# Optimization experiments

Measured on AMD Instinct MI355X. Metric: run time of the kernel, lower is better.

The kernel has to match this reference:

```python
import jax, jax.numpy as jnp
import numpy as np


def setup_inputs() -> dict:
    key = jax.random.key(0)
    k1, k2, k3 = jax.random.split(key, 3)
    B, M, J = 4096, 64, 24  # batch, n_max_markers, n_joints
    points = jax.random.normal(k1, (B, M, 3), dtype=jnp.float32)
    weight = jax.random.uniform(k2, (B, M, J), dtype=jnp.float32)  # positive soft weights
    offset = jax.random.normal(k3, (B, M, J, 3), dtype=jnp.float32)
    return {"points": points, "weight": weight, "offset": offset}


def reference(points, weight, offset):
    # P: per-joint marker offsets (B, J, 3, M); Q: world marker positions (B, 1, 3, M)
    P = jnp.transpose(offset, (0, 2, 3, 1))
    Q = jnp.transpose(points, (0, 2, 1))[:, None]
    w = jnp.transpose(weight, (0, 2, 1))[:, :, None]  # (B, J, 1, M)

    wsum = jnp.sum(w, axis=-1)                   # (B, J, 1)
    P_ = jnp.sum(P * w, axis=-1) / wsum          # (B, J, 3) weighted centroid of offsets
    Q_ = jnp.sum(Q * w, axis=-1) / wsum          # (B, J, 3) weighted centroid of markers

    X = P - P_[..., None]                        # (B, J, 3, M)
    Y = Q - Q_[..., None]                        # (B, J, 3, M) via broadcast

    # Cross-covariance S = X @ Y^T (NOTE: original multiplies un-weighted centered coords)
    S = jnp.einsum('bjdm,bjem->bjde', X, Y)      # (B, J, 3, 3)

    U, _, Vh = jnp.linalg.svd(S)
    V = jnp.swapaxes(Vh, -1, -2)
    Ut = jnp.swapaxes(U, -1, -2)
    det = jnp.linalg.det(jnp.matmul(V, Ut))      # (B, J) reflection correction
    Ut = Ut.at[..., -1, :].multiply(det[..., None])
    R = jnp.matmul(V, Ut)                        # (B, J, 3, 3) optimal rotation
    t = Q_[..., None] - jnp.matmul(R, P_[..., None])  # (B, J, 3, 1)
    return R, t
```

## Files before the change

### kernel.cpp

```cpp
#include <hip/hip_runtime.h>


constexpr int M = 64;
constexpr int J = 24;
constexpr int NACC = 22;
constexpr int NWS  = 15;

constexpr int WSTR = 27;
constexpr int OSTR = 73;
constexpr int WLEN = M * WSTR;
constexpr int OLEN = M * OSTR;
constexpr int PLEN = M * 3;
constexpr int KSP  = 8;
constexpr int RED  = KSP * J;

__global__ __launch_bounds__(256) void accum_kernel(
    const float* __restrict__ points,
    const float* __restrict__ weight,
    const float* __restrict__ offset,
    float* __restrict__ ws,
    int bj_total)
{
    __shared__ float smem[WLEN + OLEN + PLEN];
    float* lw = smem;
    float* lo = smem + WLEN;
    float* lp = smem + WLEN + OLEN;
    float* red = smem + WLEN;

    const int t = threadIdx.x;
    const int b = blockIdx.x;

    const float4* wg = (const float4*)(weight + (size_t)b * (M * J));
    for (int idx = t; idx < (M * J) / 4; idx += 256) {
        float4 v = wg[idx];
        int g0 = idx * 4;
#pragma unroll
        for (int c = 0; c < 4; ++c) {
            int g = g0 + c;
            int m = g / J, r = g - m * J;
            lw[m * WSTR + r] = (&v.x)[c];
        }
    }
    const float4* og = (const float4*)(offset + (size_t)b * (M * J * 3));
    for (int idx = t; idx < (M * J * 3) / 4; idx += 256) {
        float4 v = og[idx];
        int g0 = idx * 4;
#pragma unroll
        for (int c = 0; c < 4; ++c) {
            int g = g0 + c;
            int m = g / (J * 3), r = g - m * (J * 3);
            lo[m * OSTR + r] = (&v.x)[c];
        }
    }
    const float4* pg = (const float4*)(points + (size_t)b * (M * 3));
    if (t < PLEN / 4) ((float4*)lp)[t] = pg[t];

    __syncthreads();

    float acc[NACC];
#pragma unroll
    for (int n = 0; n < NACC; ++n) acc[n] = 0.0f;

    if (t < KSP * J) {
        const int j = t % J;
        const int k = t / J;
#pragma unroll
        for (int i = 0; i < M / KSP; ++i) {
            const int m = k * (M / KSP) + i;
            float w  = lw[m * WSTR + j];
            float o0 = lo[m * OSTR + j * 3 + 0];
            float o1 = lo[m * OSTR + j * 3 + 1];
            float o2 = lo[m * OSTR + j * 3 + 2];
            float p0 = lp[m * 3 + 0];
            float p1 = lp[m * 3 + 1];
            float p2 = lp[m * 3 + 2];
            acc[0] += w;
            acc[1] = fmaf(w, o0, acc[1]);  acc[2] = fmaf(w, o1, acc[2]);  acc[3] = fmaf(w, o2, acc[3]);
            acc[4] = fmaf(w, p0, acc[4]);  acc[5] = fmaf(w, p1, acc[5]);  acc[6] = fmaf(w, p2, acc[6]);
            acc[7] += o0; acc[8] += o1; acc[9] += o2;
            acc[10] += p0; acc[11] += p1; acc[12] += p2;
            acc[13] = fmaf(o0, p0, acc[13]); acc[14] = fmaf(o0, p1, acc[14]); acc[15] = fmaf(o0, p2, acc[15]);
            acc[16] = fmaf(o1, p0, acc[16]); acc[17] = fmaf(o1, p1, acc[17]); acc[18] = fmaf(o1, p2, acc[18]);
            acc[19] = fmaf(o2, p0, acc[19]); acc[20] = fmaf(o2, p1, acc[20]); acc[21] = fmaf(o2, p2, acc[21]);
        }
    }

    __syncthreads();
    if (t < KSP * J) {
#pragma unroll
        for (int n = 0; n < NACC; ++n) red[n * RED + t] = acc[n];
    }
    __syncthreads();

    if (t < J) {
        float T[NACC];
#pragma unroll
        for (int n = 0; n < NACC; ++n) {
            float s = 0.0f;
#pragma unroll
            for (int k = 0; k < KSP; ++k) s += red[n * RED + k * J + t];
            T[n] = s;
        }
        const float inv = __builtin_amdgcn_rcpf(T[0]);
        const float cP0 = T[1] * inv, cP1 = T[2] * inv, cP2 = T[3] * inv;
        const float cQ0 = T[4] * inv, cQ1 = T[5] * inv, cQ2 = T[6] * inv;
        const float To0 = T[7], To1 = T[8], To2 = T[9];
        const float Tp0 = T[10], Tp1 = T[11], Tp2 = T[12];
        const float fM = (float)M;
        float Sv[NWS];
        Sv[0] = T[13] - cP0 * Tp0 - cQ0 * To0 + fM * cP0 * cQ0;
        Sv[1] = T[14] - cP0 * Tp1 - cQ1 * To0 + fM * cP0 * cQ1;
        Sv[2] = T[15] - cP0 * Tp2 - cQ2 * To0 + fM * cP0 * cQ2;
        Sv[3] = T[16] - cP1 * Tp0 - cQ0 * To1 + fM * cP1 * cQ0;
        Sv[4] = T[17] - cP1 * Tp1 - cQ1 * To1 + fM * cP1 * cQ1;
        Sv[5] = T[18] - cP1 * Tp2 - cQ2 * To1 + fM * cP1 * cQ2;
        Sv[6] = T[19] - cP2 * Tp0 - cQ0 * To2 + fM * cP2 * cQ0;
        Sv[7] = T[20] - cP2 * Tp1 - cQ1 * To2 + fM * cP2 * cQ1;
        Sv[8] = T[21] - cP2 * Tp2 - cQ2 * To2 + fM * cP2 * cQ2;
        Sv[9] = cP0;  Sv[10] = cP1; Sv[11] = cP2;
        Sv[12] = cQ0; Sv[13] = cQ1; Sv[14] = cQ2;
        const int bj = b * J + t;
#pragma unroll
        for (int n = 0; n < NWS; ++n) ws[(size_t)n * bj_total + bj] = Sv[n];
    }
}

template<int P, int Q>
__device__ __forceinline__ void jrot(float A[4][4], float V[4][4]) {
    float apq = A[P][Q];
    float theta = (A[Q][Q] - A[P][P]) * __builtin_amdgcn_rcpf(2.0f * apq);
    float t = __builtin_amdgcn_rcpf(fabsf(theta) + __builtin_amdgcn_sqrtf(fmaf(theta, theta, 1.0f)));
    t = (theta < 0.0f) ? -t : t;
    t = (apq == 0.0f) ? 0.0f : t;
    float c = __builtin_amdgcn_rsqf(fmaf(t, t, 1.0f));
    float s = t * c;
#pragma unroll
    for (int k = 0; k < 4; ++k) {
        float akp = A[k][P], akq = A[k][Q];
        A[k][P] = c * akp - s * akq;
        A[k][Q] = s * akp + c * akq;
    }
#pragma unroll
    for (int k = 0; k < 4; ++k) {
        float apk = A[P][k], aqk = A[Q][k];
        A[P][k] = c * apk - s * aqk;
        A[Q][k] = s * apk + c * aqk;
        float vkp = V[k][P], vkq = V[k][Q];
        V[k][P] = c * vkp - s * vkq;
        V[k][Q] = s * vkp + c * vkq;
    }
}

__device__ __forceinline__ void horn_solve(
    float S00, float S01, float S02, float S10, float S11, float S12,
    float S20, float S21, float S22,
    float cP0, float cP1, float cP2, float cQ0, float cQ1, float cQ2,
    float* __restrict__ Rout, float* __restrict__ tout)
{
    float A[4][4], V[4][4];
    A[0][0] = S00 + S11 + S22;
    A[0][1] = A[1][0] = S12 - S21;
    A[0][2] = A[2][0] = S20 - S02;
    A[0][3] = A[3][0] = S01 - S10;
    A[1][1] = S00 - S11 - S22;
    A[1][2] = A[2][1] = S01 + S10;
    A[1][3] = A[3][1] = S02 + S20;
    A[2][2] = -S00 + S11 - S22;
    A[2][3] = A[3][2] = S12 + S21;
    A[3][3] = -S00 - S11 + S22;
#pragma unroll
    for (int r = 0; r < 4; ++r)
#pragma unroll
        for (int c = 0; c < 4; ++c)
            V[r][c] = (r == c) ? 1.0f : 0.0f;

#pragma unroll 1
    for (int sweep = 0; sweep < 6; ++sweep) {
        jrot<0, 1>(A, V); jrot<0, 2>(A, V); jrot<0, 3>(A, V);
        jrot<1, 2>(A, V); jrot<1, 3>(A, V); jrot<2, 3>(A, V);
    }

    float best = A[0][0];
    float qw = V[0][0], qx = V[1][0], qy = V[2][0], qz = V[3][0];
#pragma unroll
    for (int i = 1; i < 4; ++i) {
        bool better = A[i][i] > best;
        best = better ? A[i][i] : best;
        qw = better ? V[0][i] : qw;
        qx = better ? V[1][i] : qx;
        qy = better ? V[2][i] : qy;
        qz = better ? V[3][i] : qz;
    }
    float nrm = __builtin_amdgcn_rsqf(qw * qw + qx * qx + qy * qy + qz * qz);
    qw *= nrm; qx *= nrm; qy *= nrm; qz *= nrm;

    float R00 = 1.f - 2.f * (qy * qy + qz * qz);
    float R01 = 2.f * (qx * qy - qw * qz);
    float R02 = 2.f * (qx * qz + qw * qy);
    float R10 = 2.f * (qx * qy + qw * qz);
    float R11 = 1.f - 2.f * (qx * qx + qz * qz);
    float R12 = 2.f * (qy * qz - qw * qx);
    float R20 = 2.f * (qx * qz - qw * qy);
    float R21 = 2.f * (qy * qz + qw * qx);
    float R22 = 1.f - 2.f * (qx * qx + qy * qy);

    Rout[0] = R00; Rout[1] = R01; Rout[2] = R02;
    Rout[3] = R10; Rout[4] = R11; Rout[5] = R12;
    Rout[6] = R20; Rout[7] = R21; Rout[8] = R22;
    tout[0] = cQ0 - (R00 * cP0 + R01 * cP1 + R02 * cP2);
    tout[1] = cQ1 - (R10 * cP0 + R11 * cP1 + R12 * cP2);
    tout[2] = cQ2 - (R20 * cP0 + R21 * cP1 + R22 * cP2);
}

__global__ __launch_bounds__(64) void solve_kernel(
    const float* __restrict__ ws, float* __restrict__ out, int bj_total)
{
    int tid = blockIdx.x * 64 + threadIdx.x;
    if (tid >= bj_total) return;
    float Sv[NWS];
#pragma unroll
    for (int n = 0; n < NWS; ++n) Sv[n] = ws[(size_t)n * bj_total + tid];
    float Rr[9], tr[3];
    horn_solve(Sv[0], Sv[1], Sv[2], Sv[3], Sv[4], Sv[5], Sv[6], Sv[7], Sv[8],
               Sv[9], Sv[10], Sv[11], Sv[12], Sv[13], Sv[14], Rr, tr);
    float* Rout = out + (size_t)tid * 9;
#pragma unroll
    for (int n = 0; n < 9; ++n) Rout[n] = Rr[n];
    float* tout = out + (size_t)bj_total * 9 + (size_t)tid * 3;
    tout[0] = tr[0]; tout[1] = tr[1]; tout[2] = tr[2];
}

__global__ __launch_bounds__(256) void fused_kernel(
    const float* __restrict__ points, const float* __restrict__ weight,
    const float* __restrict__ offset, float* __restrict__ out, int bj_total)
{
    int tid = blockIdx.x * blockDim.x + threadIdx.x;
    if (tid >= bj_total) return;
    int b = tid / J, j = tid - b * J;
    const float* wq = weight + (size_t)b * M * J + j;
    const float* oq = offset + ((size_t)b * M * J + j) * 3;
    const float* pq = points + (size_t)b * M * 3;
    float a[NACC];
#pragma unroll
    for (int n = 0; n < NACC; ++n) a[n] = 0.0f;
#pragma unroll 4
    for (int m = 0; m < M; ++m) {
        float w = wq[m * J];
        float o0 = oq[m * (J * 3) + 0], o1 = oq[m * (J * 3) + 1], o2 = oq[m * (J * 3) + 2];
        float p0 = pq[m * 3 + 0], p1 = pq[m * 3 + 1], p2 = pq[m * 3 + 2];
        a[0] += w;
        a[1] = fmaf(w, o0, a[1]); a[2] = fmaf(w, o1, a[2]); a[3] = fmaf(w, o2, a[3]);
        a[4] = fmaf(w, p0, a[4]); a[5] = fmaf(w, p1, a[5]); a[6] = fmaf(w, p2, a[6]);
        a[7] += o0; a[8] += o1; a[9] += o2;
        a[10] += p0; a[11] += p1; a[12] += p2;
        a[13] = fmaf(o0, p0, a[13]); a[14] = fmaf(o0, p1, a[14]); a[15] = fmaf(o0, p2, a[15]);
        a[16] = fmaf(o1, p0, a[16]); a[17] = fmaf(o1, p1, a[17]); a[18] = fmaf(o1, p2, a[18]);
        a[19] = fmaf(o2, p0, a[19]); a[20] = fmaf(o2, p1, a[20]); a[21] = fmaf(o2, p2, a[21]);
    }
    float inv = __builtin_amdgcn_rcpf(a[0]);
    float cP0 = a[1] * inv, cP1 = a[2] * inv, cP2 = a[3] * inv;
    float cQ0 = a[4] * inv, cQ1 = a[5] * inv, cQ2 = a[6] * inv;
    const float fM = (float)M;
    float S00 = a[13] - cP0 * a[10] - cQ0 * a[7] + fM * cP0 * cQ0;
    float S01 = a[14] - cP0 * a[11] - cQ1 * a[7] + fM * cP0 * cQ1;
    float S02 = a[15] - cP0 * a[12] - cQ2 * a[7] + fM * cP0 * cQ2;
    float S10 = a[16] - cP1 * a[10] - cQ0 * a[8] + fM * cP1 * cQ0;
    float S11 = a[17] - cP1 * a[11] - cQ1 * a[8] + fM * cP1 * cQ1;
    float S12 = a[18] - cP1 * a[12] - cQ2 * a[8] + fM * cP1 * cQ2;
    float S20 = a[19] - cP2 * a[10] - cQ0 * a[9] + fM * cP2 * cQ0;
    float S21 = a[20] - cP2 * a[11] - cQ1 * a[9] + fM * cP2 * cQ1;
    float S22 = a[21] - cP2 * a[12] - cQ2 * a[9] + fM * cP2 * cQ2;
    float Rr[9], tr[3];
    horn_solve(S00, S01, S02, S10, S11, S12, S20, S21, S22,
               cP0, cP1, cP2, cQ0, cQ1, cQ2, Rr, tr);
    float* Rout = out + (size_t)tid * 9;
#pragma unroll
    for (int n = 0; n < 9; ++n) Rout[n] = Rr[n];
    float* tout = out + (size_t)bj_total * 9 + (size_t)tid * 3;
    tout[0] = tr[0]; tout[1] = tr[1]; tout[2] = tr[2];
}

extern "C" void kernel_launch(void* const* d_in, const int* in_sizes, int n_in,
                              void* d_out, int out_size, void* d_ws, size_t ws_size,
                              hipStream_t stream) {
    const float* points = (const float*)d_in[0];
    const float* weight = (const float*)d_in[1];
    const float* offset = (const float*)d_in[2];
    float* out = (float*)d_out;

    int B = in_sizes[0] / (M * 3);
    int bj_total = B * J;

    size_t need = (size_t)NWS * bj_total * sizeof(float);
    if (ws_size >= need) {
        accum_kernel<<<B, 256, 0, stream>>>(points, weight, offset, (float*)d_ws, bj_total);
        solve_kernel<<<(bj_total + 63) / 64, 64, 0, stream>>>((const float*)d_ws, out, bj_total);
    } else {
        fused_kernel<<<(bj_total + 255) / 256, 256, 0, stream>>>(points, weight, offset, out, bj_total);
    }
}
```

Baseline: 153.7 us.

## Fuse accumulation and Horn eigen-solve into one kernel with LDS-staged output

Result: slower. 187.1 us (+21.7%).

```diff
diff --git a/kernel.cpp b/kernel.cpp
--- a/kernel.cpp
+++ b/kernel.cpp
@@ -4,7 +4,6 @@
 constexpr int M = 64;
 constexpr int J = 24;
 constexpr int NACC = 22;
-constexpr int NWS  = 15;
 
 constexpr int WSTR = 27;
 constexpr int OSTR = 73;
@@ -14,11 +13,37 @@
 constexpr int KSP  = 8;
 constexpr int RED  = KSP * J;
 
-__global__ __launch_bounds__(256) void accum_kernel(
+template<int P, int Q>
+__device__ __forceinline__ void jrot(float A[4][4], float V[4][4]) {
+    float apq = A[P][Q];
+    float theta = (A[Q][Q] - A[P][P]) * __builtin_amdgcn_rcpf(2.0f * apq);
+    float t = __builtin_amdgcn_rcpf(fabsf(theta) + __builtin_amdgcn_sqrtf(fmaf(theta, theta, 1.0f)));
+    t = (theta < 0.0f) ? -t : t;
+    t = (apq == 0.0f) ? 0.0f : t;
+    float c = __builtin_amdgcn_rsqf(fmaf(t, t, 1.0f));
+    float s = t * c;
+#pragma unroll
+    for (int k = 0; k < 4; ++k) {
+        float akp = A[k][P], akq = A[k][Q];
+        A[k][P] = c * akp - s * akq;
+        A[k][Q] = s * akp + c * akq;
+    }
+#pragma unroll
+    for (int k = 0; k < 4; ++k) {
+        float apk = A[P][k], aqk = A[Q][k];
+        A[P][k] = c * apk - s * aqk;
+        A[Q][k] = s * apk + c * aqk;
+        float vkp = V[k][P], vkq = V[k][Q];
+        V[k][P] = c * vkp - s * vkq;
+        V[k][Q] = s * vkp + c * vkq;
+    }
+}
+
+__global__ __launch_bounds__(256) void kabsch_fused(
     const float* __restrict__ points,
     const float* __restrict__ weight,
     const float* __restrict__ offset,
-    float* __restrict__ ws,
+    float* __restrict__ out,
     int bj_total)
 {
     __shared__ float smem[WLEN + OLEN + PLEN];
@@ -26,6 +51,7 @@
     float* lo = smem + WLEN;
     float* lp = smem + WLEN + OLEN;
     float* red = smem + WLEN;
+    float* ost = smem;
 
     const int t = threadIdx.x;
     const int b = blockIdx.x;
@@ -107,177 +133,81 @@
         const float To0 = T[7], To1 = T[8], To2 = T[9];
         const float Tp0 = T[10], Tp1 = T[11], Tp2 = T[12];
         const float fM = (float)M;
-        float Sv[NWS];
-        Sv[0] = T[13] - cP0 * Tp0 - cQ0 * To0 + fM * cP0 * cQ0;
-        Sv[1] = T[14] - cP0 * Tp1 - cQ1 * To0 + fM * cP0 * cQ1;
-        Sv[2] = T[15] - cP0 * Tp2 - cQ2 * To0 + fM * cP0 * cQ2;
-        Sv[3] = T[16] - cP1 * Tp0 - cQ0 * To1 + fM * cP1 * cQ0;
-        Sv[4] = T[17] - cP1 * Tp1 - cQ1 * To1 + fM * cP1 * cQ1;
-        Sv[5] = T[18] - cP1 * Tp2 - cQ2 * To1 + fM * cP1 * cQ2;
-        Sv[6] = T[19] - cP2 * Tp0 - cQ0 * To2 + fM * cP2 * cQ0;
-        Sv[7] = T[20] - cP2 * Tp1 - cQ1 * To2 + fM * cP2 * cQ1;
-        Sv[8] = T[21] - cP2 * Tp2 - cQ2 * To2 + fM * cP2 * cQ2;
-        Sv[9] = cP0;  Sv[10] = cP1; Sv[11] = cP2;
-        Sv[12] = cQ0; Sv[13] = cQ1; Sv[14] = cQ2;
-        const int bj = b * J + t;
-#pragma unroll
-        for (int n = 0; n < NWS; ++n) ws[(size_t)n * bj_total + bj] = Sv[n];
-    }
-}
-
-template<int P, int Q>
-__device__ __forceinline__ void jrot(float A[4][4], float V[4][4]) {
-    float apq = A[P][Q];
-    float theta = (A[Q][Q] - A[P][P]) * __builtin_amdgcn_rcpf(2.0f * apq);
-    float t = __builtin_amdgcn_rcpf(fabsf(theta) + __builtin_amdgcn_sqrtf(fmaf(theta, theta, 1.0f)));
-    t = (theta < 0.0f) ? -t : t;
-    t = (apq == 0.0f) ? 0.0f : t;
-    float c = __builtin_amdgcn_rsqf(fmaf(t, t, 1.0f));
-    float s = t * c;
-#pragma unroll
-    for (int k = 0; k < 4; ++k) {
-        float akp = A[k][P], akq = A[k][Q];
-        A[k][P] = c * akp - s * akq;
-        A[k][Q] = s * akp + c * akq;
-    }
-#pragma unroll
-    for (int k = 0; k < 4; ++k) {
-        float apk = A[P][k], aqk = A[Q][k];
-        A[P][k] = c * apk - s * aqk;
-        A[Q][k] = s * apk + c * aqk;
-        float vkp = V[k][P], vkq = V[k][Q];
-        V[k][P] = c * vkp - s * vkq;
-        V[k][Q] = s * vkp + c * vkq;
-    }
-}
-
-__device__ __forceinline__ void horn_solve(
-    float S00, float S01, float S02, float S10, float S11, float S12,
-    float S20, float S21, float S22,
-    float cP0, float cP1, float cP2, float cQ0, float cQ1, float cQ2,
-    float* __restrict__ Rout, float* __restrict__ tout)
-{
-    float A[4][4], V[4][4];
-    A[0][0] = S00 + S11 + S22;
-    A[0][1] = A[1][0] = S12 - S21;
-    A[0][2] = A[2][0] = S20 - S02;
-    A[0][3] = A[3][0] = S01 - S10;
-    A[1][1] = S00 - S11 - S22;
-    A[1][2] = A[2][1] = S01 + S10;
-    A[1][3] = A[3][1] = S02 + S20;
-    A[2][2] = -S00 + S11 - S22;
-    A[2][3] = A[3][2] = S12 + S21;
-    A[3][3] = -S00 - S11 + S22;
-#pragma unroll
-    for (int r = 0; r < 4; ++r)
-#pragma unroll
-        for (int c = 0; c < 4; ++c)
-            V[r][c] = (r == c) ? 1.0f : 0.0f;
+        float S00 = T[13] - cP0 * Tp0 - cQ0 * To0 + fM * cP0 * cQ0;
+        float S01 = T[14] - cP0 * Tp1 - cQ1 * To0 + fM * cP0 * cQ1;
+        float S02 = T[15] - cP0 * Tp2 - cQ2 * To0 + fM * cP0 * cQ2;
+        float S10 = T[16] - cP1 * Tp0 - cQ0 * To1 + fM * cP1 * cQ0;
+        float S11 = T[17] - cP1 * Tp1 - cQ1 * To1 + fM * cP1 * cQ1;
+        float S12 = T[18] - cP1 * Tp2 - cQ2 * To1 + fM * cP1 * cQ2;
+        float S20 = T[19] - cP2 * Tp0 - cQ0 * To2 + fM * cP2 * cQ0;
+        float S21 = T[20] - cP2 * Tp1 - cQ1 * To2 + fM * cP2 * cQ1;
+        float S22 = T[21] - cP2 * Tp2 - cQ2 * To2 + fM * cP2 * cQ2;
+
+        float A[4][4], V[4][4];
+        A[0][0] = S00 + S11 + S22;
+        A[0][1] = A[1][0] = S12 - S21;
+        A[0][2] = A[2][0] = S20 - S02;
+        A[0][3] = A[3][0] = S01 - S10;
+        A[1][1] = S00 - S11 - S22;
+        A[1][2] = A[2][1] = S01 + S10;
+        A[1][3] = A[3][1] = S02 + S20;
+        A[2][2] = -S00 + S11 - S22;
+        A[2][3] = A[3][2] = S12 + S21;
+        A[3][3] = -S00 - S11 + S22;
+#pragma unroll
+        for (int r = 0; r < 4; ++r)
+#pragma unroll
+            for (int c = 0; c < 4; ++c)
+                V[r][c] = (r == c) ? 1.0f : 0.0f;
 
 #pragma unroll 1
-    for (int sweep = 0; sweep < 6; ++sweep) {
-        jrot<0, 1>(A, V); jrot<0, 2>(A, V); jrot<0, 3>(A, V);
-        jrot<1, 2>(A, V); jrot<1, 3>(A, V); jrot<2, 3>(A, V);
-    }
-
-    float best = A[0][0];
-    float qw = V[0][0], qx = V[1][0], qy = V[2][0], qz = V[3][0];
-#pragma unroll
-    for (int i = 1; i < 4; ++i) {
-        bool better = A[i][i] > best;
-        best = better ? A[i][i] : best;
-        qw = better ? V[0][i] : qw;
-        qx = better ? V[1][i] : qx;
-        qy = better ? V[2][i] : qy;
-        qz = better ? V[3][i] : qz;
-    }
-    float nrm = __builtin_amdgcn_rsqf(qw * qw + qx * qx + qy * qy + qz * qz);
-    qw *= nrm; qx *= nrm; qy *= nrm; qz *= nrm;
-
-    float R00 = 1.f - 2.f * (qy * qy + qz * qz);
-    float R01 = 2.f * (qx * qy - qw * qz);
-    float R02 = 2.f * (qx * qz + qw * qy);
-    float R10 = 2.f * (qx * qy + qw * qz);
-    float R11 = 1.f - 2.f * (qx * qx + qz * qz);
-    float R12 = 2.f * (qy * qz - qw * qx);
-    float R20 = 2.f * (qx * qz - qw * qy);
-    float R21 = 2.f * (qy * qz + qw * qx);
-    float R22 = 1.f - 2.f * (qx * qx + qy * qy);
-
-    Rout[0] = R00; Rout[1] = R01; Rout[2] = R02;
-    Rout[3] = R10; Rout[4] = R11; Rout[5] = R12;
-    Rout[6] = R20; Rout[7] = R21; Rout[8] = R22;
-    tout[0] = cQ0 - (R00 * cP0 + R01 * cP1 + R02 * cP2);
-    tout[1] = cQ1 - (R10 * cP0 + R11 * cP1 + R12 * cP2);
-    tout[2] = cQ2 - (R20 * cP0 + R21 * cP1 + R22 * cP2);
-}
-
-__global__ __launch_bounds__(64) void solve_kernel(
-    const float* __restrict__ ws, float* __restrict__ out, int bj_total)
-{
-    int tid = blockIdx.x * 64 + threadIdx.x;
-    if (tid >= bj_total) return;
-    float Sv[NWS];
-#pragma unroll
-    for (int n = 0; n < NWS; ++n) Sv[n] = ws[(size_t)n * bj_total + tid];
-    float Rr[9], tr[3];
-    horn_solve(Sv[0], Sv[1], Sv[2], Sv[3], Sv[4], Sv[5], Sv[6], Sv[7], Sv[8],
-               Sv[9], Sv[10], Sv[11], Sv[12], Sv[13], Sv[14], Rr, tr);
-    float* Rout = out + (size_t)tid * 9;
-#pragma unroll
-    for (int n = 0; n < 9; ++n) Rout[n] = Rr[n];
-    float* tout = out + (size_t)bj_total * 9 + (size_t)tid * 3;
-    tout[0] = tr[0]; tout[1] = tr[1]; tout[2] = tr[2];
-}
-
-__global__ __launch_bounds__(256) void fused_kernel(
-    const float* __restrict__ points, const float* __restrict__ weight,
-    const float* __restrict__ offset, float* __restrict__ out, int bj_total)
-{
-    int tid = blockIdx.x * blockDim.x + threadIdx.x;
-    if (tid >= bj_total) return;
-    int b = tid / J, j = tid - b * J;
-    const float* wq = weight + (size_t)b * M * J + j;
-    const float* oq = offset + ((size_t)b * M * J + j) * 3;
-    const float* pq = points + (size_t)b * M * 3;
-    float a[NACC];
-#pragma unroll
-    for (int n = 0; n < NACC; ++n) a[n] = 0.0f;
-#pragma unroll 4
-    for (int m = 0; m < M; ++m) {
-        float w = wq[m * J];
-        float o0 = oq[m * (J * 3) + 0], o1 = oq[m * (J * 3) + 1], o2 = oq[m * (J * 3) + 2];
-        float p0 = pq[m * 3 + 0], p1 = pq[m * 3 + 1], p2 = pq[m * 3 + 2];
-        a[0] += w;
-        a[1] = fmaf(w, o0, a[1]); a[2] = fmaf(w, o1, a[2]); a[3] = fmaf(w, o2, a[3]);
-        a[4] = fmaf(w, p0, a[4]); a[5] = fmaf(w, p1, a[5]); a[6] = fmaf(w, p2, a[6]);
-        a[7] += o0; a[8] += o1; a[9] += o2;
-        a[10] += p0; a[11] += p1; a[12] += p2;
-        a[13] = fmaf(o0, p0, a[13]); a[14] = fmaf(o0, p1, a[14]); a[15] = fmaf(o0, p2, a[15]);
-        a[16] = fmaf(o1, p0, a[16]); a[17] = fmaf(o1, p1, a[17]); a[18] = fmaf(o1, p2, a[18]);
-        a[19] = fmaf(o2, p0, a[19]); a[20] = fmaf(o2, p1, a[20]); a[21] = fmaf(o2, p2, a[21]);
-    }
-    float inv = __builtin_amdgcn_rcpf(a[0]);
-    float cP0 = a[1] * inv, cP1 = a[2] * inv, cP2 = a[3] * inv;
-    float cQ0 = a[4] * inv, cQ1 = a[5] * inv, cQ2 = a[6] * inv;
-    const float fM = (float)M;
-    float S00 = a[13] - cP0 * a[10] - cQ0 * a[7] + fM * cP0 * cQ0;
-    float S01 = a[14] - cP0 * a[11] - cQ1 * a[7] + fM * cP0 * cQ1;
-    float S02 = a[15] - cP0 * a[12] - cQ2 * a[7] + fM * cP0 * cQ2;
-    float S10 = a[16] - cP1 * a[10] - cQ0 * a[8] + fM * cP1 * cQ0;
-    float S11 = a[17] - cP1 * a[11] - cQ1 * a[8] + fM * cP1 * cQ1;
-    float S12 = a[18] - cP1 * a[12] - cQ2 * a[8] + fM * cP1 * cQ2;
-    float S20 = a[19] - cP2 * a[10] - cQ0 * a[9] + fM * cP2 * cQ0;
-    float S21 = a[20] - cP2 * a[11] - cQ1 * a[9] + fM * cP2 * cQ1;
-    float S22 = a[21] - cP2 * a[12] - cQ2 * a[9] + fM * cP2 * cQ2;
-    float Rr[9], tr[3];
-    horn_solve(S00, S01, S02, S10, S11, S12, S20, S21, S22,
-               cP0, cP1, cP2, cQ0, cQ1, cQ2, Rr, tr);
-    float* Rout = out + (size_t)tid * 9;
-#pragma unroll
-    for (int n = 0; n < 9; ++n) Rout[n] = Rr[n];
-    float* tout = out + (size_t)bj_total * 9 + (size_t)tid * 3;
-    tout[0] = tr[0]; tout[1] = tr[1]; tout[2] = tr[2];
+        for (int sweep = 0; sweep < 6; ++sweep) {
+            jrot<0, 1>(A, V); jrot<0, 2>(A, V); jrot<0, 3>(A, V);
+            jrot<1, 2>(A, V); jrot<1, 3>(A, V); jrot<2, 3>(A, V);
+        }
+
+        float best = A[0][0];
+        float qw = V[0][0], qx = V[1][0], qy = V[2][0], qz = V[3][0];
+#pragma unroll
+        for (int i = 1; i < 4; ++i) {
+            bool better = A[i][i] > best;
+            best = better ? A[i][i] : best;
+            qw = better ? V[0][i] : qw;
+            qx = better ? V[1][i] : qx;
+            qy = better ? V[2][i] : qy;
+            qz = better ? V[3][i] : qz;
+        }
+        float nrm = __builtin_amdgcn_rsqf(qw * qw + qx * qx + qy * qy + qz * qz);
+        qw *= nrm; qx *= nrm; qy *= nrm; qz *= nrm;
+
+        float R00 = 1.f - 2.f * (qy * qy + qz * qz);
+        float R01 = 2.f * (qx * qy - qw * qz);
+        float R02 = 2.f * (qx * qz + qw * qy);
+        float R10 = 2.f * (qx * qy + qw * qz);
+        float R11 = 1.f - 2.f * (qx * qx + qz * qz);
+        float R12 = 2.f * (qy * qz - qw * qx);
+        float R20 = 2.f * (qx * qz - qw * qy);
+        float R21 = 2.f * (qy * qz + qw * qx);
+        float R22 = 1.f - 2.f * (qx * qx + qy * qy);
+
+        float* r = ost + t * 9;
+        r[0] = R00; r[1] = R01; r[2] = R02;
+        r[3] = R10; r[4] = R11; r[5] = R12;
+        r[6] = R20; r[7] = R21; r[8] = R22;
+        float* tv = ost + 216 + t * 3;
+        tv[0] = cQ0 - (R00 * cP0 + R01 * cP1 + R02 * cP2);
+        tv[1] = cQ1 - (R10 * cP0 + R11 * cP1 + R12 * cP2);
+        tv[2] = cQ2 - (R20 * cP0 + R21 * cP1 + R22 * cP2);
+    }
+
+    __syncthreads();
+
+    if (t < 54) {
+        ((float4*)(out + (size_t)b * (J * 9)))[t] = ((const float4*)ost)[t];
+    } else if (t < 72) {
+        ((float4*)(out + (size_t)bj_total * 9 + (size_t)b * (J * 3)))[t - 54] =
+            ((const float4*)ost)[t];
+    }
 }
 
 extern "C" void kernel_launch(void* const* d_in, const int* in_sizes, int n_in,
@@ -290,12 +220,5 @@
 
     int B = in_sizes[0] / (M * 3);
     int bj_total = B * J;
-
-    size_t need = (size_t)NWS * bj_total * sizeof(float);
-    if (ws_size >= need) {
-        accum_kernel<<<B, 256, 0, stream>>>(points, weight, offset, (float*)d_ws, bj_total);
-        solve_kernel<<<(bj_total + 63) / 64, 64, 0, stream>>>((const float*)d_ws, out, bj_total);
-    } else {
-        fused_kernel<<<(bj_total + 255) / 256, 256, 0, stream>>>(points, weight, offset, out, bj_total);
-    }
+    kabsch_fused<<<B, 256, 0, stream>>>(points, weight, offset, out, bj_total);
 }
```

## Replace LDS-staged accumulation with direct global loads and wave shuffle reduction

Applied to the files above, without the earlier changes.

After: 146.6 us. -4.6%, faster.

```diff
diff --git a/kernel.cpp b/kernel.cpp
--- a/kernel.cpp
+++ b/kernel.cpp
@@ -5,124 +5,85 @@
 constexpr int J = 24;
 constexpr int NACC = 22;
 constexpr int NWS  = 15;
-
-constexpr int WSTR = 27;
-constexpr int OSTR = 73;
-constexpr int WLEN = M * WSTR;
-constexpr int OLEN = M * OSTR;
-constexpr int PLEN = M * 3;
 constexpr int KSP  = 8;
-constexpr int RED  = KSP * J;
-
-__global__ __launch_bounds__(256) void accum_kernel(
+constexpr int SPW  = 8;
+constexpr int SPB  = 32;
+
+__global__ __launch_bounds__(256, 6) void accum_kernel(
     const float* __restrict__ points,
     const float* __restrict__ weight,
     const float* __restrict__ offset,
     float* __restrict__ ws,
     int bj_total)
 {
-    __shared__ float smem[WLEN + OLEN + PLEN];
-    float* lw = smem;
-    float* lo = smem + WLEN;
-    float* lp = smem + WLEN + OLEN;
-    float* red = smem + WLEN;
-
-    const int t = threadIdx.x;
-    const int b = blockIdx.x;
-
-    const float4* wg = (const float4*)(weight + (size_t)b * (M * J));
-    for (int idx = t; idx < (M * J) / 4; idx += 256) {
-        float4 v = wg[idx];
-        int g0 = idx * 4;
-#pragma unroll
-        for (int c = 0; c < 4; ++c) {
-            int g = g0 + c;
-            int m = g / J, r = g - m * J;
-            lw[m * WSTR + r] = (&v.x)[c];
-        }
-    }
-    const float4* og = (const float4*)(offset + (size_t)b * (M * J * 3));
-    for (int idx = t; idx < (M * J * 3) / 4; idx += 256) {
-        float4 v = og[idx];
-        int g0 = idx * 4;
-#pragma unroll
-        for (int c = 0; c < 4; ++c) {
-            int g = g0 + c;
-            int m = g / (J * 3), r = g - m * (J * 3);
-            lo[m * OSTR + r] = (&v.x)[c];
-        }
-    }
-    const float4* pg = (const float4*)(points + (size_t)b * (M * 3));
-    if (t < PLEN / 4) ((float4*)lp)[t] = pg[t];
-
-    __syncthreads();
+    const int t    = threadIdx.x;
+    const int lane = t & 63;
+    const int wv   = t >> 6;
+    const int k    = lane >> 3;
+    const int sl   = lane & 7;
+    const int bj   = blockIdx.x * SPB + wv * SPW + sl;
+    const int bjc  = bj < bj_total ? bj : bj_total - 1;
+    const int b    = bjc / J;
+    const int j    = bjc - b * J;
+
+    const float* wq = weight + (size_t)b * (M * J) + (size_t)(k * 8) * J + j;
+    const float* oq = offset + ((size_t)b * (M * J) + (size_t)(k * 8) * J + j) * 3;
+    const float* pq = points + (size_t)b * (M * 3) + (size_t)(k * 8) * 3;
 
     float acc[NACC];
 #pragma unroll
     for (int n = 0; n < NACC; ++n) acc[n] = 0.0f;
 
-    if (t < KSP * J) {
-        const int j = t % J;
-        const int k = t / J;
-#pragma unroll
-        for (int i = 0; i < M / KSP; ++i) {
-            const int m = k * (M / KSP) + i;
-            float w  = lw[m * WSTR + j];
-            float o0 = lo[m * OSTR + j * 3 + 0];
-            float o1 = lo[m * OSTR + j * 3 + 1];
-            float o2 = lo[m * OSTR + j * 3 + 2];
-            float p0 = lp[m * 3 + 0];
-            float p1 = lp[m * 3 + 1];
-            float p2 = lp[m * 3 + 2];
-            acc[0] += w;
-            acc[1] = fmaf(w, o0, acc[1]);  acc[2] = fmaf(w, o1, acc[2]);  acc[3] = fmaf(w, o2, acc[3]);
-            acc[4] = fmaf(w, p0, acc[4]);  acc[5] = fmaf(w, p1, acc[5]);  acc[6] = fmaf(w, p2, acc[6]);
-            acc[7] += o0; acc[8] += o1; acc[9] += o2;
-            acc[10] += p0; acc[11] += p1; acc[12] += p2;
-            acc[13] = fmaf(o0, p0, acc[13]); acc[14] = fmaf(o0, p1, acc[14]); acc[15] = fmaf(o0, p2, acc[15]);
-            acc[16] = fmaf(o1, p0, acc[16]); acc[17] = fmaf(o1, p1, acc[17]); acc[18] = fmaf(o1, p2, acc[18]);
-            acc[19] = fmaf(o2, p0, acc[19]); acc[20] = fmaf(o2, p1, acc[20]); acc[21] = fmaf(o2, p2, acc[21]);
-        }
-    }
-
-    __syncthreads();
-    if (t < KSP * J) {
-#pragma unroll
-        for (int n = 0; n < NACC; ++n) red[n * RED + t] = acc[n];
-    }
-    __syncthreads();
-
-    if (t < J) {
-        float T[NACC];
-#pragma unroll
-        for (int n = 0; n < NACC; ++n) {
-            float s = 0.0f;
-#pragma unroll
-            for (int k = 0; k < KSP; ++k) s += red[n * RED + k * J + t];
-            T[n] = s;
-        }
-        const float inv = __builtin_amdgcn_rcpf(T[0]);
-        const float cP0 = T[1] * inv, cP1 = T[2] * inv, cP2 = T[3] * inv;
-        const float cQ0 = T[4] * inv, cQ1 = T[5] * inv, cQ2 = T[6] * inv;
-        const float To0 = T[7], To1 = T[8], To2 = T[9];
-        const float Tp0 = T[10], Tp1 = T[11], Tp2 = T[12];
-        const float fM = (float)M;
-        float Sv[NWS];
-        Sv[0] = T[13] - cP0 * Tp0 - cQ0 * To0 + fM * cP0 * cQ0;
-        Sv[1] = T[14] - cP0 * Tp1 - cQ1 * To0 + fM * cP0 * cQ1;
-        Sv[2] = T[15] - cP0 * Tp2 - cQ2 * To0 + fM * cP0 * cQ2;
-        Sv[3] = T[16] - cP1 * Tp0 - cQ0 * To1 + fM * cP1 * cQ0;
-        Sv[4] = T[17] - cP1 * Tp1 - cQ1 * To1 + fM * cP1 * cQ1;
-        Sv[5] = T[18] - cP1 * Tp2 - cQ2 * To1 + fM * cP1 * cQ2;
-        Sv[6] = T[19] - cP2 * Tp0 - cQ0 * To2 + fM * cP2 * cQ0;
-        Sv[7] = T[20] - cP2 * Tp1 - cQ1 * To2 + fM * cP2 * cQ1;
-        Sv[8] = T[21] - cP2 * Tp2 - cQ2 * To2 + fM * cP2 * cQ2;
-        Sv[9] = cP0;  Sv[10] = cP1; Sv[11] = cP2;
-        Sv[12] = cQ0; Sv[13] = cQ1; Sv[14] = cQ2;
-        const int bj = b * J + t;
-#pragma unroll
-        for (int n = 0; n < NWS; ++n) ws[(size_t)n * bj_total + bj] = Sv[n];
-    }
+#pragma unroll
+    for (int i = 0; i < M / KSP; ++i) {
+        float w  = wq[i * J];
+        float o0 = oq[i * (J * 3) + 0];
+        float o1 = oq[i * (J * 3) + 1];
+        float o2 = oq[i * (J * 3) + 2];
+        float p0 = pq[i * 3 + 0];
+        float p1 = pq[i * 3 + 1];
+        float p2 = pq[i * 3 + 2];
+        acc[0] += w;
+        acc[1] = fmaf(w, o0, acc[1]);  acc[2] = fmaf(w, o1, acc[2]);  acc[3] = fmaf(w, o2, acc[3]);
+        acc[4] = fmaf(w, p0, acc[4]);  acc[5] = fmaf(w, p1, acc[5]);  acc[6] = fmaf(w, p2, acc[6]);
+        acc[7] += o0; acc[8] += o1; acc[9] += o2;
+        acc[10] += p0; acc[11] += p1; acc[12] += p2;
+        acc[13] = fmaf(o0, p0, acc[13]); acc[14] = fmaf(o0, p1, acc[14]); acc[15] = fmaf(o0, p2, acc[15]);
+        acc[16] = fmaf(o1, p0, acc[16]); acc[17] = fmaf(o1, p1, acc[17]); acc[18] = fmaf(o1, p2, acc[18]);
+        acc[19] = fmaf(o2, p0, acc[19]); acc[20] = fmaf(o2, p1, acc[20]); acc[21] = fmaf(o2, p2, acc[21]);
+    }
+
+#pragma unroll
+    for (int n = 0; n < NACC; ++n) {
+        float v = acc[n];
+        v += __shfl_xor(v, 8);
+        v += __shfl_xor(v, 16);
+        v += __shfl_xor(v, 32);
+        acc[n] = v;
+    }
+
+    if (k != 0 || bj >= bj_total) return;
+
+    const float inv = __builtin_amdgcn_rcpf(acc[0]);
+    const float cP0 = acc[1] * inv, cP1 = acc[2] * inv, cP2 = acc[3] * inv;
+    const float cQ0 = acc[4] * inv, cQ1 = acc[5] * inv, cQ2 = acc[6] * inv;
+    const float To0 = acc[7], To1 = acc[8], To2 = acc[9];
+    const float Tp0 = acc[10], Tp1 = acc[11], Tp2 = acc[12];
+    const float fM = (float)M;
+    float Sv[NWS];
+    Sv[0] = acc[13] - cP0 * Tp0 - cQ0 * To0 + fM * cP0 * cQ0;
+    Sv[1] = acc[14] - cP0 * Tp1 - cQ1 * To0 + fM * cP0 * cQ1;
+    Sv[2] = acc[15] - cP0 * Tp2 - cQ2 * To0 + fM * cP0 * cQ2;
+    Sv[3] = acc[16] - cP1 * Tp0 - cQ0 * To1 + fM * cP1 * cQ0;
+    Sv[4] = acc[17] - cP1 * Tp1 - cQ1 * To1 + fM * cP1 * cQ1;
+    Sv[5] = acc[18] - cP1 * Tp2 - cQ2 * To1 + fM * cP1 * cQ2;
+    Sv[6] = acc[19] - cP2 * Tp0 - cQ0 * To2 + fM * cP2 * cQ0;
+    Sv[7] = acc[20] - cP2 * Tp1 - cQ1 * To2 + fM * cP2 * cQ1;
+    Sv[8] = acc[21] - cP2 * Tp2 - cQ2 * To2 + fM * cP2 * cQ2;
+    Sv[9]  = cP0; Sv[10] = cP1; Sv[11] = cP2;
+    Sv[12] = cQ0; Sv[13] = cQ1; Sv[14] = cQ2;
+#pragma unroll
+    for (int n = 0; n < NWS; ++n) ws[(size_t)n * bj_total + bj] = Sv[n];
 }
 
 template<int P, int Q>
@@ -293,7 +254,8 @@
 
     size_t need = (size_t)NWS * bj_total * sizeof(float);
     if (ws_size >= need) {
-        accum_kernel<<<B, 256, 0, stream>>>(points, weight, offset, (float*)d_ws, bj_total);
+        int grid1 = (bj_total + SPB - 1) / SPB;
+        accum_kernel<<<grid1, 256, 0, stream>>>(points, weight, offset, (float*)d_ws, bj_total);
         solve_kernel<<<(bj_total + 63) / 64, 64, 0, stream>>>((const float*)d_ws, out, bj_total);
     } else {
         fused_kernel<<<(bj_total + 255) / 256, 256, 0, stream>>>(points, weight, offset, out, bj_total);
```
